# Performance work log

Hardware: AMD Instinct MI355X
Metric: run time of the kernel (lower is better)

The kernel has to match this reference:

```python
import jax, jax.numpy as jnp
import numpy as np

N_HEAD = 16
EMBED = 1024
HEAD_DIM = EMBED // N_HEAD  # 64
HALF = HEAD_DIM // 2        # 32
T = 2048                    # total packed tokens
NSEG = 4
SEG = T // NSEG             # 512 tokens per packed sequence
SCALE = HEAD_DIM ** -0.5


def _apply_rotary_vision(t, freqs):
    # t: [T, H, D], freqs: [T, D/2] -> Qwen2-VL style vision RoPE
    cos = jnp.concatenate([jnp.cos(freqs), jnp.cos(freqs)], axis=-1)[:, None, :]  # [T,1,D]
    sin = jnp.concatenate([jnp.sin(freqs), jnp.sin(freqs)], axis=-1)[:, None, :]
    t1, t2 = t[..., :HALF], t[..., HALF:]
    rot = jnp.concatenate([-t2, t1], axis=-1)  # rotate_half
    return t * cos + rot * sin


def setup_inputs() -> dict:
    key = jax.random.key(0)
    k1, k2, k3, k4, k5 = jax.random.split(key, 5)
    hidden_states = jax.random.normal(k1, (T, EMBED), dtype=jnp.float32)
    cu_seqlens = (jnp.arange(NSEG + 1, dtype=jnp.int32) * SEG)  # [0,512,...,2048]
    # realistic rotary freqs: position within each segment * inverse frequencies
    pos = jnp.tile(jnp.arange(SEG, dtype=jnp.float32), NSEG)  # [T]
    inv_freq = 1.0 / (10000.0 ** (jnp.arange(HALF, dtype=jnp.float32) / HALF))
    rotary_pos_emb = pos[:, None] * inv_freq[None, :]  # [T, HALF]
    std = 0.02
    wq = jax.random.normal(k2, (EMBED, EMBED), dtype=jnp.float32) * std
    wk = jax.random.normal(k3, (EMBED, EMBED), dtype=jnp.float32) * std
    wv = jax.random.normal(k4, (EMBED, EMBED), dtype=jnp.float32) * std
    wo = jax.random.normal(k5, (EMBED, EMBED), dtype=jnp.float32) * std
    return {"hidden_states": hidden_states, "cu_seqlens": cu_seqlens,
            "rotary_pos_emb": rotary_pos_emb, "wq": wq, "wk": wk, "wv": wv, "wo": wo}


def reference(hidden_states, cu_seqlens, rotary_pos_emb, wq, wk, wv, wo):
    # QKV projections (nn.Linear, bias=False): y = x @ W.T
    q = (hidden_states @ wq.T).reshape(T, N_HEAD, HEAD_DIM)
    k = (hidden_states @ wk.T).reshape(T, N_HEAD, HEAD_DIM)
    v = (hidden_states @ wv.T).reshape(T, N_HEAD, HEAD_DIM)
    q = _apply_rotary_vision(q, rotary_pos_emb)
    k = _apply_rotary_vision(k, rotary_pos_emb)
    # varlen (block-diagonal, non-causal) attention over packed segments
    seg_id = jnp.searchsorted(cu_seqlens, jnp.arange(T, dtype=cu_seqlens.dtype), side='right')
    same_seg = seg_id[:, None] == seg_id[None, :]  # [T, T]
    scores = jnp.einsum('thd,shd->hts', q, k) * SCALE  # [H, T, T]
    scores = jnp.where(same_seg[None, :, :], scores, jnp.finfo(scores.dtype).min)
    probs = jax.nn.softmax(scores, axis=-1)
    attn = jnp.einsum('hts,shd->thd', probs, v).reshape(T, EMBED)
    return attn @ wo.T
```

## Files before the change

kernel.cpp:

```cpp
#include <hip/hip_runtime.h>
#include <cstdint>

#define T_TOK 2048
#define EMBED 1024
#define NH    16
#define HD    64
#define HALF  32
#define SEG   512
#define SL    (0.125f * 1.44269504088896f)

typedef __attribute__((ext_vector_type(8))) __bf16 bf16x8;
typedef __attribute__((ext_vector_type(4))) float  f32x4;
typedef unsigned short u16;
typedef unsigned int   u32;

__device__ __forceinline__ u16 f2bf(float f) {
  u32 u = __builtin_bit_cast(u32, f);
  u += 0x7fffu + ((u >> 16) & 1u);
  return (u16)(u >> 16);
}

__device__ __forceinline__ void gld_lds16(const void* g, void* l) {
  __builtin_amdgcn_global_load_lds(
      reinterpret_cast<__attribute__((address_space(1))) u32*>(
          reinterpret_cast<uintptr_t>(g)),
      reinterpret_cast<__attribute__((address_space(3))) u32*>(
          reinterpret_cast<uintptr_t>(l)),
      16, 0, 0);
}

__global__ __launch_bounds__(256) void convert_k(
    const float* __restrict__ H,  const float* __restrict__ wq,
    const float* __restrict__ wk, const float* __restrict__ wv,
    const float* __restrict__ wo, u16* __restrict__ dst) {
  const size_t gid = (size_t)blockIdx.x * 256 + threadIdx.x;
  const size_t e = gid * 4;
  const float* src; size_t off;
  const size_t HN = (size_t)T_TOK * EMBED;
  if (e < HN) { src = H; off = e; }
  else {
    size_t r = e - HN;
    int w = (int)(r >> 20);
    off = r & ((1u << 20) - 1);
    src = (w == 0) ? wq : (w == 1) ? wk : (w == 2) ? wv : wo;
  }
  const float4 v = *(const float4*)(src + off);
  ushort4 o;
  o.x = f2bf(v.x); o.y = f2bf(v.y); o.z = f2bf(v.z); o.w = f2bf(v.w);
  *(ushort4*)(dst + e) = o;
}

__global__ __launch_bounds__(256) void qkv_k(
    const u16* __restrict__ Hb, const u16* __restrict__ Wb,
    const float* __restrict__ rope, u16* __restrict__ Qb,
    u16* __restrict__ Khh, u16* __restrict__ Vss) {
  constexpr int K = 1024, N = 1024;
  __shared__ alignas(16) u16 As[2][2][128 * 32];
  __shared__ alignas(16) u16 Bs[2][2][128 * 32];
  const int tid = threadIdx.x;
  const int wave = tid >> 6, lane = tid & 63;
  const int quad = lane >> 4, l16 = lane & 15;
  const int bm = blockIdx.y * 128, bn = blockIdx.x * 128;
  const int z = blockIdx.z;
  const u16* Bz = Wb + ((size_t)z << 20);
  const int wm = (wave >> 1) * 64, wn = (wave & 1) * 64;

  f32x4 acc[4][4];
#pragma unroll
  for (int i = 0; i < 4; ++i)
#pragma unroll
    for (int j = 0; j < 4; ++j) { f32x4 zz = {0.f, 0.f, 0.f, 0.f}; acc[i][j] = zz; }

  const int srow = tid >> 2, scol = (tid & 3) * 8;
  const u16* gA = Hb + (size_t)(bm + srow) * K + scol;
  const u16* gB = Bz + (size_t)(bn + srow) * K + scol;

#pragma unroll
  for (int p = 0; p < 2; ++p)
#pragma unroll
    for (int hrow = 0; hrow < 2; ++hrow) {
      gld_lds16(gA + (size_t)hrow * 64 * K + p * 32,
                (char*)&As[0][p][0] + hrow * 4096 + wave * 1024);
      gld_lds16(gB + (size_t)hrow * 64 * K + p * 32,
                (char*)&Bs[0][p][0] + hrow * 4096 + wave * 1024);
    }

  for (int kk = 0; kk < K; kk += 64) {
    __syncthreads();
    const int cur = (kk >> 6) & 1, nxt = cur ^ 1;
    if (kk + 64 < K) {
      const int kn = kk + 64;
#pragma unroll
      for (int p = 0; p < 2; ++p)
#pragma unroll
        for (int hrow = 0; hrow < 2; ++hrow) {
          gld_lds16(gA + (size_t)hrow * 64 * K + kn + p * 32,
                    (char*)&As[nxt][p][0] + hrow * 4096 + wave * 1024);
          gld_lds16(gB + (size_t)hrow * 64 * K + kn + p * 32,
                    (char*)&Bs[nxt][p][0] + hrow * 4096 + wave * 1024);
        }
    }
#pragma unroll
    for (int p = 0; p < 2; ++p) {
      const u16* Ac = &As[cur][p][0];
      const u16* Bc = &Bs[cur][p][0];
      bf16x8 af[4], bfv[4];
#pragma unroll
      for (int i = 0; i < 4; ++i)
        af[i] = *(const bf16x8*)(Ac + (wm + i * 16 + l16) * 32 + quad * 8);
#pragma unroll
      for (int j = 0; j < 4; ++j)
        bfv[j] = *(const bf16x8*)(Bc + (wn + j * 16 + l16) * 32 + quad * 8);
#pragma unroll
      for (int i = 0; i < 4; ++i)
#pragma unroll
        for (int j = 0; j < 4; ++j)
          acc[i][j] = __builtin_amdgcn_mfma_f32_16x16x32_bf16(af[i], bfv[j],
                                                              acc[i][j], 0, 0, 0);
    }
  }

  const int h = (bn + wn) >> 6;
  if (z == 0) {
#pragma unroll
    for (int i = 0; i < 4; ++i)
#pragma unroll
      for (int r = 0; r < 4; ++r) {
        const int t = bm + wm + i * 16 + quad * 4 + r;
        const float f0 = rope[t * HALF + l16];
        const float f1 = rope[t * HALF + 16 + l16];
        float s0, c0, s1, c1;
        __sincosf(f0, &s0, &c0);
        __sincosf(f1, &s1, &c1);
        const float v0 = acc[i][0][r], v1 = acc[i][1][r];
        const float v2 = acc[i][2][r], v3 = acc[i][3][r];
        const size_t base = (size_t)t * N + bn + wn + l16;
        Qb[base]      = f2bf(v0 * c0 - v2 * s0);
        Qb[base + 16] = f2bf(v1 * c1 - v3 * s1);
        Qb[base + 32] = f2bf(v2 * c0 + v0 * s0);
        Qb[base + 48] = f2bf(v3 * c1 + v1 * s1);
      }
  } else if (z == 1) {
#pragma unroll
    for (int i = 0; i < 4; ++i)
#pragma unroll
      for (int r = 0; r < 4; ++r) {
        const int t = bm + wm + i * 16 + quad * 4 + r;
        const float f0 = rope[t * HALF + l16];
        const float f1 = rope[t * HALF + 16 + l16];
        float s0, c0, s1, c1;
        __sincosf(f0, &s0, &c0);
        __sincosf(f1, &s1, &c1);
        const float v0 = acc[i][0][r], v1 = acc[i][1][r];
        const float v2 = acc[i][2][r], v3 = acc[i][3][r];
        const size_t b0 = ((size_t)(h * 2 + 0) * T_TOK + t) * 32;
        const size_t b1 = ((size_t)(h * 2 + 1) * T_TOK + t) * 32;
        Khh[b0 + l16]      = f2bf(v0 * c0 - v2 * s0);
        Khh[b0 + 16 + l16] = f2bf(v1 * c1 - v3 * s1);
        Khh[b1 + l16]      = f2bf(v2 * c0 + v0 * s0);
        Khh[b1 + 16 + l16] = f2bf(v3 * c1 + v1 * s1);
      }
  } else {
#pragma unroll
    for (int i = 0; i < 4; ++i) {
      const int t0 = bm + wm + i * 16 + quad * 4;
      const int tp = t0 >> 5, toff = t0 & 31;
#pragma unroll
      for (int j = 0; j < 4; ++j) {
        const int d = j * 16 + l16;
        ushort4 pk;
        pk.x = f2bf(acc[i][j][0]); pk.y = f2bf(acc[i][j][1]);
        pk.z = f2bf(acc[i][j][2]); pk.w = f2bf(acc[i][j][3]);
        *(ushort4*)(Vss + ((size_t)(h * 64 + tp) * 64 + d) * 32 + toff) = pk;
      }
    }
  }
}

__global__ __launch_bounds__(256) void attn_st(
    const u16* __restrict__ Qb, const u16* __restrict__ Khh,
    const u16* __restrict__ Vss, u16* __restrict__ Ab) {
  const int b = blockIdx.x;
  const int qt = b & 7, seg = (b >> 3) & 3, h = b >> 5;
  const int tid = threadIdx.x;
  const int wave = tid >> 6, lane = tid & 63;
  const int quad = lane >> 4, l16 = lane & 15;

  __shared__ alignas(16) u16 Ks[2][64 * 32];
  __shared__ alignas(16) u16 Vs[2][64 * 32];
  __shared__ alignas(16) u16 Pl[4][16 * 72];

  const int qbase = seg * SEG + qt * 64 + wave * 16;
  const u16* qp = Qb + (size_t)(qbase + l16) * EMBED + h * HD + quad * 8;
  const bf16x8 qf0 = *(const bf16x8*)qp;
  const bf16x8 qf1 = *(const bf16x8*)(qp + 32);

  const u16* Ksrc0 = Khh + ((size_t)(h * 2 + 0) * T_TOK + seg * SEG) * 32;
  const u16* Ksrc1 = Khh + ((size_t)(h * 2 + 1) * T_TOK + seg * SEG) * 32;
  const u16* Vsrc  = Vss + ((size_t)(h * 64 + seg * 16) * 64) * 32;

  float lsum[4] = {0.f, 0.f, 0.f, 0.f};
  f32x4 O[4];
#pragma unroll
  for (int nt = 0; nt < 4; ++nt) { f32x4 z = {0.f, 0.f, 0.f, 0.f}; O[nt] = z; }

  u16* pw = Pl[wave];
  const int toff = tid * 8;

  uint4 kreg0 = *(const uint4*)(Ksrc0 + toff);
  uint4 kreg1 = *(const uint4*)(Ksrc1 + toff);
  uint4 vreg0 = *(const uint4*)(Vsrc + toff);
  uint4 vreg1 = *(const uint4*)(Vsrc + 2048 + toff);

  for (int cc = 0; cc < 8; ++cc) {
    *(uint4*)((char*)&Ks[0][0] + tid * 16) = kreg0;
    *(uint4*)((char*)&Ks[1][0] + tid * 16) = kreg1;
    *(uint4*)((char*)&Vs[0][0] + tid * 16) = vreg0;
    *(uint4*)((char*)&Vs[1][0] + tid * 16) = vreg1;
    __syncthreads();
    if (cc + 1 < 8) {
      const size_t kc = (size_t)(cc + 1) * 2048 + toff;
      const size_t vc = (size_t)(cc + 1) * 4096 + toff;
      kreg0 = *(const uint4*)(Ksrc0 + kc);
      kreg1 = *(const uint4*)(Ksrc1 + kc);
      vreg0 = *(const uint4*)(Vsrc + vc);
      vreg1 = *(const uint4*)(Vsrc + vc + 2048);
    }
    f32x4 S[4];
#pragma unroll
    for (int kt = 0; kt < 4; ++kt) {
      const bf16x8 k0 = *(const bf16x8*)&Ks[0][(kt * 16 + l16) * 32 + quad * 8];
      const bf16x8 k1 = *(const bf16x8*)&Ks[1][(kt * 16 + l16) * 32 + quad * 8];
      f32x4 s = {0.f, 0.f, 0.f, 0.f};
      s = __builtin_amdgcn_mfma_f32_16x16x32_bf16(qf0, k0, s, 0, 0, 0);
      s = __builtin_amdgcn_mfma_f32_16x16x32_bf16(qf1, k1, s, 0, 0, 0);
      S[kt] = s;
    }
    bf16x8 vf0[4], vf1[4];
#pragma unroll
    for (int nt = 0; nt < 4; ++nt) {
      vf0[nt] = *(const bf16x8*)&Vs[0][(nt * 16 + l16) * 32 + quad * 8];
      vf1[nt] = *(const bf16x8*)&Vs[1][(nt * 16 + l16) * 32 + quad * 8];
    }
    float ps[4] = {0.f, 0.f, 0.f, 0.f};
#pragma unroll
    for (int kt = 0; kt < 4; ++kt)
#pragma unroll
      for (int r = 0; r < 4; ++r) {
        float p = exp2f(S[kt][r] * SL);
        ps[r] += p;
        pw[(quad * 4 + r) * 72 + kt * 16 + l16] = f2bf(p);
      }
#pragma unroll
    for (int r = 0; r < 4; ++r) lsum[r] += ps[r];
    const u16* pp = pw + l16 * 72 + quad * 8;
    const bf16x8 pf0 = *(const bf16x8*)pp;
    const bf16x8 pf1 = *(const bf16x8*)(pp + 32);
#pragma unroll
    for (int nt = 0; nt < 4; ++nt) {
      O[nt] = __builtin_amdgcn_mfma_f32_16x16x32_bf16(pf0, vf0[nt], O[nt], 0, 0, 0);
      O[nt] = __builtin_amdgcn_mfma_f32_16x16x32_bf16(pf1, vf1[nt], O[nt], 0, 0, 0);
    }
    __syncthreads();
  }
#pragma unroll
  for (int r = 0; r < 4; ++r) {
    float l = lsum[r];
#pragma unroll
    for (int off = 1; off < 16; off <<= 1) l += __shfl_xor(l, off);
    lsum[r] = 1.f / l;
  }
#pragma unroll
  for (int nt = 0; nt < 4; ++nt)
#pragma unroll
    for (int r = 0; r < 4; ++r) {
      const int trow = qbase + quad * 4 + r;
      Ab[(size_t)trow * EMBED + h * HD + nt * 16 + l16] = f2bf(O[nt][r] * lsum[r]);
    }
}

__global__ __launch_bounds__(256) void oproj_k(
    const u16* __restrict__ Ab, const u16* __restrict__ Wo,
    float* __restrict__ out) {
  constexpr int K = 1024, N = 1024;
  __shared__ alignas(16) u16 As[2][2][64 * 32];
  __shared__ alignas(16) u16 Bs[2][2][64 * 32];
  const int tid = threadIdx.x;
  const int wave = tid >> 6, lane = tid & 63;
  const int quad = lane >> 4, l16 = lane & 15;
  const int bm = blockIdx.y * 64, bn = blockIdx.x * 64;

  f32x4 acc[4];
#pragma unroll
  for (int j = 0; j < 4; ++j) { f32x4 z = {0.f, 0.f, 0.f, 0.f}; acc[j] = z; }

  const int srow = tid >> 2, scol = (tid & 3) * 8;
  const u16* gA = Ab + (size_t)(bm + srow) * K + scol;
  const u16* gB = Wo + (size_t)(bn + srow) * K + scol;

#pragma unroll
  for (int p = 0; p < 2; ++p) {
    gld_lds16(gA + p * 32, (char*)&As[0][p][0] + wave * 1024);
    gld_lds16(gB + p * 32, (char*)&Bs[0][p][0] + wave * 1024);
  }

  for (int kk = 0; kk < K; kk += 64) {
    __syncthreads();
    const int cur = (kk >> 6) & 1, nxt = cur ^ 1;
    if (kk + 64 < K) {
      const int kn = kk + 64;
#pragma unroll
      for (int p = 0; p < 2; ++p) {
        gld_lds16(gA + kn + p * 32, (char*)&As[nxt][p][0] + wave * 1024);
        gld_lds16(gB + kn + p * 32, (char*)&Bs[nxt][p][0] + wave * 1024);
      }
    }
#pragma unroll
    for (int p = 0; p < 2; ++p) {
      const u16* Ac = &As[cur][p][0];
      const u16* Bc = &Bs[cur][p][0];
      const bf16x8 af = *(const bf16x8*)(Ac + (wave * 16 + l16) * 32 + quad * 8);
      bf16x8 bfv[4];
#pragma unroll
      for (int j = 0; j < 4; ++j)
        bfv[j] = *(const bf16x8*)(Bc + (j * 16 + l16) * 32 + quad * 8);
#pragma unroll
      for (int j = 0; j < 4; ++j)
        acc[j] = __builtin_amdgcn_mfma_f32_16x16x32_bf16(af, bfv[j],
                                                         acc[j], 0, 0, 0);
    }
  }

#pragma unroll
  for (int r = 0; r < 4; ++r) {
    const int row = bm + wave * 16 + quad * 4 + r;
#pragma unroll
    for (int j = 0; j < 4; ++j)
      out[(size_t)row * N + bn + j * 16 + l16] = acc[j][r];
  }
}

extern "C" void kernel_launch(void* const* d_in, const int* in_sizes, int n_in,
                              void* d_out, int out_size, void* d_ws,
                              size_t ws_size, hipStream_t stream) {
  const float* H    = (const float*)d_in[0];
  const float* rope = (const float*)d_in[2];
  const float* wq   = (const float*)d_in[3];
  const float* wk   = (const float*)d_in[4];
  const float* wv   = (const float*)d_in[5];
  const float* wo   = (const float*)d_in[6];
  float* out        = (float*)d_out;

  constexpr size_t M1 = (size_t)1 << 20;
  if (ws_size < 28 * M1) return;

  u16* ws16 = (u16*)d_ws;
  u16* Hb  = ws16;
  u16* Wb  = ws16 + 2 * M1;
  u16* Qb  = ws16 + 6 * M1;
  u16* Khh = ws16 + 8 * M1;
  u16* Vss = ws16 + 10 * M1;
  u16* Ab  = ws16 + 12 * M1;

  convert_k<<<6144, 256, 0, stream>>>(H, wq, wk, wv, wo, ws16);
  qkv_k<<<dim3(8, 16, 3), 256, 0, stream>>>(Hb, Wb, rope, Qb, Khh, Vss);
  attn_st<<<512, 256, 0, stream>>>(Qb, Khh, Vss, Ab);
  oproj_k<<<dim3(16, 32), 256, 0, stream>>>(Ab, Wb + 3 * M1, out);
}
```

Measured before the change: 126.2 us.

## Double-buffer K/V in LDS and use 128-query blocks in attention

The attention kernel now launches 256 blocks of 512 threads, each covering 128 queries instead of 64, so every K/V chunk staged in LDS is reused by eight waves instead of four. K/V tiles are double-buffered in shared memory with a register prefetch two chunks ahead, which leaves one barrier per iteration instead of two. The aim is to halve redundant K/V global traffic and let LDS staging overlap the MFMA compute. In exchange the grid has fewer blocks on a large GPU, LDS per block doubles, and each thread issues narrower 8-byte loads.

```diff
diff --git a/kernel.cpp b/kernel.cpp
--- a/kernel.cpp
+++ b/kernel.cpp
@@ -177,20 +177,20 @@
   }
 }
 
-__global__ __launch_bounds__(256) void attn_st(
+__global__ __launch_bounds__(512) void attn_st(
     const u16* __restrict__ Qb, const u16* __restrict__ Khh,
     const u16* __restrict__ Vss, u16* __restrict__ Ab) {
   const int b = blockIdx.x;
-  const int qt = b & 7, seg = (b >> 3) & 3, h = b >> 5;
+  const int qt = b & 3, seg = (b >> 2) & 3, h = b >> 4;
   const int tid = threadIdx.x;
   const int wave = tid >> 6, lane = tid & 63;
   const int quad = lane >> 4, l16 = lane & 15;
 
-  __shared__ alignas(16) u16 Ks[2][64 * 32];
-  __shared__ alignas(16) u16 Vs[2][64 * 32];
-  __shared__ alignas(16) u16 Pl[4][16 * 72];
-
-  const int qbase = seg * SEG + qt * 64 + wave * 16;
+  __shared__ alignas(16) u16 Ks[2][2][64 * 32];
+  __shared__ alignas(16) u16 Vs[2][2][64 * 32];
+  __shared__ alignas(16) u16 Pl[8][16 * 72];
+
+  const int qbase = seg * SEG + qt * 128 + wave * 16;
   const u16* qp = Qb + (size_t)(qbase + l16) * EMBED + h * HD + quad * 8;
   const bf16x8 qf0 = *(const bf16x8*)qp;
   const bf16x8 qf1 = *(const bf16x8*)(qp + 32);
@@ -205,32 +205,31 @@
   for (int nt = 0; nt < 4; ++nt) { f32x4 z = {0.f, 0.f, 0.f, 0.f}; O[nt] = z; }
 
   u16* pw = Pl[wave];
-  const int toff = tid * 8;
-
-  uint4 kreg0 = *(const uint4*)(Ksrc0 + toff);
-  uint4 kreg1 = *(const uint4*)(Ksrc1 + toff);
-  uint4 vreg0 = *(const uint4*)(Vsrc + toff);
-  uint4 vreg1 = *(const uint4*)(Vsrc + 2048 + toff);
-
+  const int toff = tid * 4;
+
+  uint2 kreg0 = *(const uint2*)(Ksrc0 + toff);
+  uint2 kreg1 = *(const uint2*)(Ksrc1 + toff);
+  uint2 vreg0 = *(const uint2*)(Vsrc + toff);
+  uint2 vreg1 = *(const uint2*)(Vsrc + 2048 + toff);
+  *(uint2*)((char*)&Ks[0][0][0] + tid * 8) = kreg0;
+  *(uint2*)((char*)&Ks[0][1][0] + tid * 8) = kreg1;
+  *(uint2*)((char*)&Vs[0][0][0] + tid * 8) = vreg0;
+  *(uint2*)((char*)&Vs[0][1][0] + tid * 8) = vreg1;
+  kreg0 = *(const uint2*)(Ksrc0 + 2048 + toff);
+  kreg1 = *(const uint2*)(Ksrc1 + 2048 + toff);
+  vreg0 = *(const uint2*)(Vsrc + 4096 + toff);
+  vreg1 = *(const uint2*)(Vsrc + 4096 + 2048 + toff);
+  asm volatile("s_waitcnt lgkmcnt(0)" ::: "memory");
+  __builtin_amdgcn_s_barrier();
+  __builtin_amdgcn_sched_barrier(0);
+
+  int cur = 0;
   for (int cc = 0; cc < 8; ++cc) {
-    *(uint4*)((char*)&Ks[0][0] + tid * 16) = kreg0;
-    *(uint4*)((char*)&Ks[1][0] + tid * 16) = kreg1;
-    *(uint4*)((char*)&Vs[0][0] + tid * 16) = vreg0;
-    *(uint4*)((char*)&Vs[1][0] + tid * 16) = vreg1;
-    __syncthreads();
-    if (cc + 1 < 8) {
-      const size_t kc = (size_t)(cc + 1) * 2048 + toff;
-      const size_t vc = (size_t)(cc + 1) * 4096 + toff;
-      kreg0 = *(const uint4*)(Ksrc0 + kc);
-      kreg1 = *(const uint4*)(Ksrc1 + kc);
-      vreg0 = *(const uint4*)(Vsrc + vc);
-      vreg1 = *(const uint4*)(Vsrc + vc + 2048);
-    }
     f32x4 S[4];
 #pragma unroll
     for (int kt = 0; kt < 4; ++kt) {
-      const bf16x8 k0 = *(const bf16x8*)&Ks[0][(kt * 16 + l16) * 32 + quad * 8];
-      const bf16x8 k1 = *(const bf16x8*)&Ks[1][(kt * 16 + l16) * 32 + quad * 8];
+      const bf16x8 k0 = *(const bf16x8*)&Ks[cur][0][(kt * 16 + l16) * 32 + quad * 8];
+      const bf16x8 k1 = *(const bf16x8*)&Ks[cur][1][(kt * 16 + l16) * 32 + quad * 8];
       f32x4 s = {0.f, 0.f, 0.f, 0.f};
       s = __builtin_amdgcn_mfma_f32_16x16x32_bf16(qf0, k0, s, 0, 0, 0);
       s = __builtin_amdgcn_mfma_f32_16x16x32_bf16(qf1, k1, s, 0, 0, 0);
@@ -239,8 +238,8 @@
     bf16x8 vf0[4], vf1[4];
 #pragma unroll
     for (int nt = 0; nt < 4; ++nt) {
-      vf0[nt] = *(const bf16x8*)&Vs[0][(nt * 16 + l16) * 32 + quad * 8];
-      vf1[nt] = *(const bf16x8*)&Vs[1][(nt * 16 + l16) * 32 + quad * 8];
+      vf0[nt] = *(const bf16x8*)&Vs[cur][0][(nt * 16 + l16) * 32 + quad * 8];
+      vf1[nt] = *(const bf16x8*)&Vs[cur][1][(nt * 16 + l16) * 32 + quad * 8];
     }
     float ps[4] = {0.f, 0.f, 0.f, 0.f};
 #pragma unroll
@@ -261,7 +260,25 @@
       O[nt] = __builtin_amdgcn_mfma_f32_16x16x32_bf16(pf0, vf0[nt], O[nt], 0, 0, 0);
       O[nt] = __builtin_amdgcn_mfma_f32_16x16x32_bf16(pf1, vf1[nt], O[nt], 0, 0, 0);
     }
-    __syncthreads();
+    if (cc < 7) {
+      const int nxt = cur ^ 1;
+      *(uint2*)((char*)&Ks[nxt][0][0] + tid * 8) = kreg0;
+      *(uint2*)((char*)&Ks[nxt][1][0] + tid * 8) = kreg1;
+      *(uint2*)((char*)&Vs[nxt][0][0] + tid * 8) = vreg0;
+      *(uint2*)((char*)&Vs[nxt][1][0] + tid * 8) = vreg1;
+      if (cc < 6) {
+        const size_t kc = (size_t)(cc + 2) * 2048 + toff;
+        const size_t vc = (size_t)(cc + 2) * 4096 + toff;
+        kreg0 = *(const uint2*)(Ksrc0 + kc);
+        kreg1 = *(const uint2*)(Ksrc1 + kc);
+        vreg0 = *(const uint2*)(Vsrc + vc);
+        vreg1 = *(const uint2*)(Vsrc + vc + 2048);
+      }
+      asm volatile("s_waitcnt lgkmcnt(0)" ::: "memory");
+      __builtin_amdgcn_s_barrier();
+      __builtin_amdgcn_sched_barrier(0);
+    }
+    cur ^= 1;
   }
 #pragma unroll
   for (int r = 0; r < 4; ++r) {
@@ -364,6 +381,6 @@
 
   convert_k<<<6144, 256, 0, stream>>>(H, wq, wk, wv, wo, ws16);
   qkv_k<<<dim3(8, 16, 3), 256, 0, stream>>>(Hb, Wb, rope, Qb, Khh, Vss);
-  attn_st<<<512, 256, 0, stream>>>(Qb, Khh, Vss, Ab);
+  attn_st<<<256, 512, 0, stream>>>(Qb, Khh, Vss, Ab);
   oproj_k<<<dim3(16, 32), 256, 0, stream>>>(Ab, Wb + 3 * M1, out);
 }
```

After: 123.1 us. -2.4%, faster.
